# Kernel tuning notes

Measured on AMD Instinct MI355X. Metric: run time of the kernel, lower is better.

## Reference

```python
import jax, jax.numpy as jnp
import numpy as np

N = 8192      # num_nodes
B = 16        # batch
IN_DIM = 2    # input_dim
HID = 64      # hid_dim
K = 2         # diffusion_steps
DEG = 16
E = N * DEG
F = IN_DIM + HID            # concat(input, state) feature dim
NUM_MAT = 2 * K + 1         # dual random walk: 2 matrices * K steps + identity


def _spmm(vals, rows, cols, x):
    # sparse [N,N] @ dense [N,M]: y[rows[e]] += vals[e] * x[cols[e]]
    return jax.ops.segment_sum(vals[:, None] * x[cols], rows, num_segments=N)


def _diff_conv(x, W, b, edge_src, edge_dst, vals1, vals2):
    # x: [B, N, F] -> [B, N*out_dim]; Chebyshev-like diffusion recursion
    x0 = jnp.transpose(x, (1, 2, 0)).reshape(N, F * B)  # [N, F*B]
    xs = [x0]
    # matrix 1 = D_out^-1 A (edges src->dst), matrix 2 = D_in^-1 A^T (edges dst->src)
    for rows, cols, vals in ((edge_src, edge_dst, vals1), (edge_dst, edge_src, vals2)):
        x1 = _spmm(vals, rows, cols, x0)
        xs.append(x1)
        xp, xc = x0, x1
        for _ in range(2, K + 1):
            xn = 2.0 * _spmm(vals, rows, cols, xc) - xp
            xs.append(xn)
            xp, xc = xc, xn
    xstk = jnp.stack(xs, 0).reshape(NUM_MAT, N, F, B)
    xstk = jnp.transpose(xstk, (3, 1, 2, 0)).reshape(B * N, F * NUM_MAT)
    out = xstk @ W + b  # [B*N, out_dim]
    return out.reshape(B, -1)


def setup_inputs() -> dict:
    key = jax.random.key(0)
    k = jax.random.split(key, 8)
    inputs = jax.random.normal(k[0], (B, N * IN_DIM), jnp.float32)
    state = jax.random.normal(k[1], (B, N * HID), jnp.float32)
    edge_src = jax.random.randint(k[2], (E,), 0, N)
    edge_dst = jax.random.randint(k[3], (E,), 0, N)
    a = jax.random.uniform(k[4], (E,), jnp.float32) + 0.1  # positive edge weights
    dout = jax.ops.segment_sum(a, edge_src, num_segments=N)
    din = jax.ops.segment_sum(a, edge_dst, num_segments=N)
    vals1 = a / jnp.where(dout > 0, dout, 1.0)[edge_src]  # random-walk normalize A
    vals2 = a / jnp.where(din > 0, din, 1.0)[edge_dst]    # random-walk normalize A^T
    std_g = 1.414 * np.sqrt(2.0 / (F * NUM_MAT + 2 * HID)).astype(np.float32)
    std_c = 1.414 * np.sqrt(2.0 / (F * NUM_MAT + HID)).astype(np.float32)
    W_gate = jax.random.normal(k[5], (F * NUM_MAT, 2 * HID), jnp.float32) * std_g
    b_gate = jnp.zeros((2 * HID,), jnp.float32)
    W_cand = jax.random.normal(k[6], (F * NUM_MAT, HID), jnp.float32) * std_c
    b_cand = jnp.zeros((HID,), jnp.float32)
    return dict(inputs=inputs, state=state, edge_src=edge_src, edge_dst=edge_dst,
                vals1=vals1, vals2=vals2, W_gate=W_gate, b_gate=b_gate,
                W_cand=W_cand, b_cand=b_cand)


def reference(inputs, state, edge_src, edge_dst, vals1, vals2,
              W_gate, b_gate, W_cand, b_cand):
    i = inputs.reshape(B, N, IN_DIM)
    s = state.reshape(B, N, HID)
    x = jnp.concatenate([i, s], axis=2)  # [B, N, F]
    value = jax.nn.sigmoid(_diff_conv(x, W_gate, b_gate, edge_src, edge_dst, vals1, vals2))
    value = value.reshape(B, N, 2 * HID)
    r = value[..., :HID].reshape(B, N * HID)
    u = value[..., HID:].reshape(B, N * HID)
    rs = (r * state).reshape(B, N, HID)
    xc = jnp.concatenate([i, rs], axis=2)
    c = jnp.tanh(_diff_conv(xc, W_cand, b_cand, edge_src, edge_dst, vals1, vals2))
    new_state = u * state + (1.0 - u) * c
    return (new_state, new_state)
```

## Files before the change

kernel.cpp:

```cpp
#include <hip/hip_runtime.h>
#include <cstddef>
#include <cstdint>

#define NNODES 8192
#define BATCH  16
#define FDIM   66
#define HID    64
#define CCH    1056
#define NEDGE  131072
#define NFB    8650752
#define SN     524288
#define OUTHALF 8388608
#define KPAD   352
#define LDA    360
#define GN     8

typedef __attribute__((ext_vector_type(8))) short bf16x8;
typedef __attribute__((ext_vector_type(4))) float f32x4;

static __device__ __forceinline__ float bf2f(ushort u) {
    union { uint32_t i; float f; } c; c.i = ((uint32_t)u) << 16; return c.f;
}
static __device__ __forceinline__ ushort f2bf(float f) {
    union { float f; uint32_t i; } c; c.f = f;
    uint32_t lsb = (c.i >> 16) & 1;
    return (ushort)((c.i + 0x7fffu + lsb) >> 16);
}


__global__ void zero_counts_kernel(int* __restrict__ c1, int* __restrict__ c2) {
    int i = blockIdx.x * 256 + threadIdx.x;
    if (i < NNODES) { c1[i] = 0; c2[i] = 0; }
}

__global__ void hist_kernel(const int* __restrict__ src, const int* __restrict__ dst,
                            int* __restrict__ c1, int* __restrict__ c2) {
    int e = blockIdx.x * 256 + threadIdx.x;
    if (e < NEDGE) {
        atomicAdd(&c1[src[e]], 1);
        atomicAdd(&c2[dst[e]], 1);
    }
}

__global__ __launch_bounds__(1024) void scan_kernel(const int* __restrict__ counts,
                                                    int* __restrict__ rowptr,
                                                    int* __restrict__ cursor) {
    __shared__ int sh[1024];
    int tid = threadIdx.x;
    int base = tid * 8;
    int local[8];
    int sum = 0;
#pragma unroll
    for (int j = 0; j < 8; ++j) { local[j] = counts[base + j]; sum += local[j]; }
    sh[tid] = sum;
    __syncthreads();
    for (int off = 1; off < 1024; off <<= 1) {
        int v = (tid >= off) ? sh[tid - off] : 0;
        __syncthreads();
        sh[tid] += v;
        __syncthreads();
    }
    int p = sh[tid] - sum;
#pragma unroll
    for (int j = 0; j < 8; ++j) {
        cursor[base + j] = p;
        p += local[j];
        rowptr[base + j + 1] = p;
    }
    if (tid == 0) rowptr[0] = 0;
}

__global__ void scatter_kernel(const int* __restrict__ src, const int* __restrict__ dst,
                               const float* __restrict__ v1, const float* __restrict__ v2,
                               int* __restrict__ cur1, int* __restrict__ cur2,
                               int* __restrict__ cols1, float* __restrict__ valsC1,
                               int* __restrict__ cols2, float* __restrict__ valsC2) {
    int e = blockIdx.x * 256 + threadIdx.x;
    if (e < NEDGE) {
        int r1 = src[e];
        int p1 = atomicAdd(&cur1[r1], 1);
        cols1[p1] = dst[e];
        valsC1[p1] = v1[e];
        int r2 = dst[e];
        int p2 = atomicAdd(&cur2[r2], 1);
        cols2[p2] = src[e];
        valsC2[p2] = v2[e];
    }
}


__global__ void convert_w_kernel(const float* __restrict__ Wg, const float* __restrict__ Wc,
                                 ushort* __restrict__ WgT, ushort* __restrict__ WcT) {
    int i = blockIdx.x * 256 + threadIdx.x;
    if (i >= 192 * KPAD) return;
    int col = i / KPAD, kk = i - col * KPAD;
    if (col < 128) {
        WgT[col * KPAD + kk] = (kk < 330) ? f2bf(Wg[kk * 128 + col]) : (ushort)0;
    } else {
        int c = col - 128;
        WcT[c * KPAD + kk] = (kk < 330) ? f2bf(Wc[kk * 64 + c]) : (ushort)0;
    }
}


__global__ void build_x0_kernel(const float* __restrict__ inputs, const float* __restrict__ state,
                                ushort* __restrict__ X0) {
    int idx = blockIdx.x * 256 + threadIdx.x;
    if (idx >= NFB) return;
    int b = idx & 15;
    int t = idx >> 4;
    int f = t % FDIM;
    int n = t / FDIM;
    float v;
    if (f < 2) v = inputs[(size_t)b * (NNODES * 2) + n * 2 + f];
    else       v = state[(size_t)b * SN + n * HID + (f - 2)];
    X0[idx] = f2bf(v);
}


static __device__ __forceinline__ void fma8(float* acc, uint4 d, float v) {
    acc[0] += v * bf2f((ushort)(d.x));  acc[1] += v * bf2f((ushort)(d.x >> 16));
    acc[2] += v * bf2f((ushort)(d.y));  acc[3] += v * bf2f((ushort)(d.y >> 16));
    acc[4] += v * bf2f((ushort)(d.z));  acc[5] += v * bf2f((ushort)(d.z >> 16));
    acc[6] += v * bf2f((ushort)(d.w));  acc[7] += v * bf2f((ushort)(d.w >> 16));
}

static __device__ __forceinline__ uint4 blend_pack8(const float* acc, uint4 p,
                                                    float alpha, float beta) {
    float o[8];
    o[0] = alpha * acc[0] + beta * bf2f((ushort)(p.x));
    o[1] = alpha * acc[1] + beta * bf2f((ushort)(p.x >> 16));
    o[2] = alpha * acc[2] + beta * bf2f((ushort)(p.y));
    o[3] = alpha * acc[3] + beta * bf2f((ushort)(p.y >> 16));
    o[4] = alpha * acc[4] + beta * bf2f((ushort)(p.z));
    o[5] = alpha * acc[5] + beta * bf2f((ushort)(p.z >> 16));
    o[6] = alpha * acc[6] + beta * bf2f((ushort)(p.w));
    o[7] = alpha * acc[7] + beta * bf2f((ushort)(p.w >> 16));
    uint4 r;
    r.x = (uint32_t)f2bf(o[0]) | ((uint32_t)f2bf(o[1]) << 16);
    r.y = (uint32_t)f2bf(o[2]) | ((uint32_t)f2bf(o[3]) << 16);
    r.z = (uint32_t)f2bf(o[4]) | ((uint32_t)f2bf(o[5]) << 16);
    r.w = (uint32_t)f2bf(o[6]) | ((uint32_t)f2bf(o[7]) << 16);
    return r;
}

__global__ __launch_bounds__(128) void spmm_kernel(const int* __restrict__ rowptr,
                                                   const int* __restrict__ cols,
                                                   const float* __restrict__ vals,
                                                   const ushort* __restrict__ x,
                                                   const ushort* __restrict__ xp,
                                                   ushort* __restrict__ y,
                                                   float alpha, float beta) {
    int n = blockIdx.x;
    int t = threadIdx.x;
    int s = rowptr[n], e = rowptr[n + 1];
    float a0[8] = {0, 0, 0, 0, 0, 0, 0, 0};
    float a1[8] = {0, 0, 0, 0, 0, 0, 0, 0};
    bool tail = t < 4;
    for (int i = s; i < e; ++i) {
        float v = vals[i];
        int c = cols[i];
        const uint4* xb = (const uint4*)(x + (size_t)c * CCH);
        fma8(a0, xb[t], v);
        if (tail) fma8(a1, xb[128 + t], v);
    }
    uint4* yb = (uint4*)(y + (size_t)n * CCH);
    const uint4* xpb = (const uint4*)(xp + (size_t)n * CCH);
    uint4 p0 = (beta != 0.f) ? xpb[t] : make_uint4(0, 0, 0, 0);
    yb[t] = blend_pack8(a0, p0, alpha, beta);
    if (tail) {
        uint4 p1 = (beta != 0.f) ? xpb[128 + t] : make_uint4(0, 0, 0, 0);
        yb[128 + t] = blend_pack8(a1, p1, alpha, beta);
    }
}


__global__ __launch_bounds__(256) void gate_mfma(const ushort* __restrict__ Xb,
                                                 const ushort* __restrict__ WgT,
                                                 const float* __restrict__ bg,
                                                 const float* __restrict__ state,
                                                 float* __restrict__ U,
                                                 ushort* __restrict__ X0mut) {
    __shared__ __align__(16) ushort At[16 * LDA];
    int tid = threadIdx.x;
    int wave = tid >> 6, lane = tid & 63;
    int row = lane & 15, quad = lane >> 4;
    int c0 = (wave * 2) * 16 + row;
    int c1 = (wave * 2 + 1) * 16 + row;

    bf16x8 w0[11], w1[11];
#pragma unroll
    for (int k = 0; k < 11; ++k) {
        w0[k] = *(const bf16x8*)(WgT + (size_t)c0 * KPAD + k * 32 + quad * 8);
        w1[k] = *(const bf16x8*)(WgT + (size_t)c1 * KPAD + k * 32 + quad * 8);
    }
    float bias0 = bg[c0], bias1 = bg[c1];

    for (int p = tid; p < 16 * 22; p += 256) {
        int b = p / 22, kk = 330 + p % 22;
        At[b * LDA + kk] = 0;
    }

    int nodeBase = blockIdx.x * GN;
    for (int g = 0; g < GN; ++g) {
        int n = nodeBase + g;
        __syncthreads();
        for (int p = tid; p < 2640; p += 256) {
            int m = p / 528;
            int r2 = p - m * 528;
            int f = r2 >> 3;
            int bp = r2 & 7;
            uint d = *(const uint*)(Xb + (size_t)m * NFB + (size_t)n * CCH + f * 16 + bp * 2);
            int kk = f * 5 + m;
            int b = bp * 2;
            At[b * LDA + kk] = (ushort)d;
            At[(b + 1) * LDA + kk] = (ushort)(d >> 16);
        }
        __syncthreads();

        f32x4 acc0 = {0.f, 0.f, 0.f, 0.f};
        f32x4 acc1 = {0.f, 0.f, 0.f, 0.f};
#pragma unroll
        for (int k = 0; k < 11; ++k) {
            bf16x8 av = *(const bf16x8*)(At + row * LDA + k * 32 + quad * 8);
            acc0 = __builtin_amdgcn_mfma_f32_16x16x32_bf16(av, w0[k], acc0, 0, 0, 0);
            acc1 = __builtin_amdgcn_mfma_f32_16x16x32_bf16(av, w1[k], acc1, 0, 0, 0);
        }
#pragma unroll
        for (int r = 0; r < 4; ++r) {
            int b = quad * 4 + r;
            float v0 = 1.f / (1.f + __expf(-(acc0[r] + bias0)));
            float v1 = 1.f / (1.f + __expf(-(acc1[r] + bias1)));
            if (wave < 2) {
                float s0 = state[(size_t)b * SN + n * HID + c0];
                float s1 = state[(size_t)b * SN + n * HID + c1];
                X0mut[(size_t)n * CCH + (2 + c0) * 16 + b] = f2bf(v0 * s0);
                X0mut[(size_t)n * CCH + (2 + c1) * 16 + b] = f2bf(v1 * s1);
            } else {
                U[(size_t)b * SN + n * HID + (c0 - HID)] = v0;
                U[(size_t)b * SN + n * HID + (c1 - HID)] = v1;
            }
        }
    }
}


__global__ __launch_bounds__(256) void cand_mfma(const ushort* __restrict__ Xb,
                                                 const ushort* __restrict__ WcT,
                                                 const float* __restrict__ bc,
                                                 const float* __restrict__ state,
                                                 const float* __restrict__ U,
                                                 float* __restrict__ out) {
    __shared__ __align__(16) ushort At[16 * LDA];
    int tid = threadIdx.x;
    int wave = tid >> 6, lane = tid & 63;
    int row = lane & 15, quad = lane >> 4;
    int c = wave * 16 + row;

    bf16x8 w[11];
#pragma unroll
    for (int k = 0; k < 11; ++k)
        w[k] = *(const bf16x8*)(WcT + (size_t)c * KPAD + k * 32 + quad * 8);
    float bias = bc[c];

    for (int p = tid; p < 16 * 22; p += 256) {
        int b = p / 22, kk = 330 + p % 22;
        At[b * LDA + kk] = 0;
    }

    int nodeBase = blockIdx.x * GN;
    for (int g = 0; g < GN; ++g) {
        int n = nodeBase + g;
        __syncthreads();
        for (int p = tid; p < 2640; p += 256) {
            int m = p / 528;
            int r2 = p - m * 528;
            int f = r2 >> 3;
            int bp = r2 & 7;
            uint d = *(const uint*)(Xb + (size_t)m * NFB + (size_t)n * CCH + f * 16 + bp * 2);
            int kk = f * 5 + m;
            int b = bp * 2;
            At[b * LDA + kk] = (ushort)d;
            At[(b + 1) * LDA + kk] = (ushort)(d >> 16);
        }
        __syncthreads();

        f32x4 acc = {0.f, 0.f, 0.f, 0.f};
#pragma unroll
        for (int k = 0; k < 11; ++k) {
            bf16x8 av = *(const bf16x8*)(At + row * LDA + k * 32 + quad * 8);
            acc = __builtin_amdgcn_mfma_f32_16x16x32_bf16(av, w[k], acc, 0, 0, 0);
        }
#pragma unroll
        for (int r = 0; r < 4; ++r) {
            int b = quad * 4 + r;
            float pre = acc[r] + bias;
            float cv = 1.f - 2.f / (__expf(2.f * pre) + 1.f);
            size_t idx = (size_t)b * SN + n * HID + c;
            float uv = U[idx];
            float s = state[idx];
            float ns = uv * s + (1.f - uv) * cv;
            out[idx] = ns;
            out[OUTHALF + idx] = ns;
        }
    }
}


extern "C" void kernel_launch(void* const* d_in, const int* in_sizes, int n_in,
                              void* d_out, int out_size, void* d_ws, size_t ws_size,
                              hipStream_t stream) {
    const float* inputs = (const float*)d_in[0];
    const float* state  = (const float*)d_in[1];
    const int*   esrc   = (const int*)d_in[2];
    const int*   edst   = (const int*)d_in[3];
    const float* v1     = (const float*)d_in[4];
    const float* v2     = (const float*)d_in[5];
    const float* Wg     = (const float*)d_in[6];
    const float* bg     = (const float*)d_in[7];
    const float* Wc     = (const float*)d_in[8];
    const float* bc     = (const float*)d_in[9];
    float* out = (float*)d_out;

    char* ws = (char*)d_ws;
    size_t off = 0;
    auto alloc = [&](size_t bytes) -> void* {
        void* p = ws + off;
        off += (bytes + 255) & ~(size_t)255;
        return p;
    };
    ushort* Xb     = (ushort*)alloc((size_t)5 * NFB * 2);
    float*  U      = (float*)alloc((size_t)OUTHALF * 4);
    ushort* WgT    = (ushort*)alloc((size_t)128 * KPAD * 2);
    ushort* WcT    = (ushort*)alloc((size_t)64 * KPAD * 2);
    int*   counts1 = (int*)alloc(NNODES * 4);
    int*   counts2 = (int*)alloc(NNODES * 4);
    int*   rowptr1 = (int*)alloc((NNODES + 1) * 4);
    int*   rowptr2 = (int*)alloc((NNODES + 1) * 4);
    int*   cursor1 = (int*)alloc(NNODES * 4);
    int*   cursor2 = (int*)alloc(NNODES * 4);
    int*   cols1   = (int*)alloc(NEDGE * 4);
    int*   cols2   = (int*)alloc(NEDGE * 4);
    float* valsC1  = (float*)alloc(NEDGE * 4);
    float* valsC2  = (float*)alloc(NEDGE * 4);

    ushort* X0 = Xb;
    ushort* X1 = Xb + (size_t)1 * NFB;
    ushort* X2 = Xb + (size_t)2 * NFB;
    ushort* X3 = Xb + (size_t)3 * NFB;
    ushort* X4 = Xb + (size_t)4 * NFB;

    zero_counts_kernel<<<(NNODES + 255) / 256, 256, 0, stream>>>(counts1, counts2);
    hist_kernel<<<(NEDGE + 255) / 256, 256, 0, stream>>>(esrc, edst, counts1, counts2);
    scan_kernel<<<1, 1024, 0, stream>>>(counts1, rowptr1, cursor1);
    scan_kernel<<<1, 1024, 0, stream>>>(counts2, rowptr2, cursor2);
    scatter_kernel<<<(NEDGE + 255) / 256, 256, 0, stream>>>(esrc, edst, v1, v2,
                                                            cursor1, cursor2,
                                                            cols1, valsC1, cols2, valsC2);

    convert_w_kernel<<<(192 * KPAD + 255) / 256, 256, 0, stream>>>(Wg, Wc, WgT, WcT);
    build_x0_kernel<<<(NFB + 255) / 256, 256, 0, stream>>>(inputs, state, X0);

    spmm_kernel<<<NNODES, 128, 0, stream>>>(rowptr1, cols1, valsC1, X0, X0, X1, 1.f, 0.f);
    spmm_kernel<<<NNODES, 128, 0, stream>>>(rowptr1, cols1, valsC1, X1, X0, X2, 2.f, -1.f);
    spmm_kernel<<<NNODES, 128, 0, stream>>>(rowptr2, cols2, valsC2, X0, X0, X3, 1.f, 0.f);
    spmm_kernel<<<NNODES, 128, 0, stream>>>(rowptr2, cols2, valsC2, X3, X0, X4, 2.f, -1.f);

    gate_mfma<<<NNODES / GN, 256, 0, stream>>>(Xb, WgT, bg, state, U, X0);

    spmm_kernel<<<NNODES, 128, 0, stream>>>(rowptr1, cols1, valsC1, X0, X0, X1, 1.f, 0.f);
    spmm_kernel<<<NNODES, 128, 0, stream>>>(rowptr1, cols1, valsC1, X1, X0, X2, 2.f, -1.f);
    spmm_kernel<<<NNODES, 128, 0, stream>>>(rowptr2, cols2, valsC2, X0, X0, X3, 1.f, 0.f);
    spmm_kernel<<<NNODES, 128, 0, stream>>>(rowptr2, cols2, valsC2, X3, X0, X4, 2.f, -1.f);

    cand_mfma<<<NNODES / GN, 256, 0, stream>>>(Xb, WcT, bc, state, U, out);
}
```

Before: 628.2 us.

## Store diffusion features batch-major per node so MFMA reads operands directly

Reorders the diffusion feature storage into node-interleaved, batch-major slabs (feature dim padded to 72) and permutes the weight K order to match. The gate and candidate MFMA kernels can then load A fragments straight from global memory, dropping the LDS transpose and its barriers. It also unrolls the SpMM edge loop by two, adds a separate buffer for the reset-scaled state, and places the U buffer in the second half of the output. The cost is padding, which adds memory traffic (the SpMM tail now covers 16 threads instead of 4), and more complex indexing.

```diff
diff --git a/kernel.cpp b/kernel.cpp
--- a/kernel.cpp
+++ b/kernel.cpp
@@ -4,15 +4,16 @@
 
 #define NNODES 8192
 #define BATCH  16
-#define FDIM   66
 #define HID    64
-#define CCH    1056
 #define NEDGE  131072
-#define NFB    8650752
 #define SN     524288
 #define OUTHALF 8388608
-#define KPAD   352
-#define LDA    360
+#define FP2    72
+#define SLABU  1152
+#define NSTR   5760
+#define NSTR4  720
+#define XCS4   144
+#define KP2    384
 #define GN     8
 
 typedef __attribute__((ext_vector_type(8))) short bf16x8;
@@ -92,29 +93,41 @@
 __global__ void convert_w_kernel(const float* __restrict__ Wg, const float* __restrict__ Wc,
                                  ushort* __restrict__ WgT, ushort* __restrict__ WcT) {
     int i = blockIdx.x * 256 + threadIdx.x;
-    if (i >= 192 * KPAD) return;
-    int col = i / KPAD, kk = i - col * KPAD;
+    if (i >= 192 * KP2) return;
+    int col = i / KP2, k2 = i - col * KP2;
+    int m = k2 / FP2, f = k2 - m * FP2;
+    bool valid = (m < 5) && (f < 66);
+    int ko = f * 5 + m;
     if (col < 128) {
-        WgT[col * KPAD + kk] = (kk < 330) ? f2bf(Wg[kk * 128 + col]) : (ushort)0;
+        WgT[col * KP2 + k2] = valid ? f2bf(Wg[ko * 128 + col]) : (ushort)0;
     } else {
         int c = col - 128;
-        WcT[c * KPAD + kk] = (kk < 330) ? f2bf(Wc[kk * 64 + c]) : (ushort)0;
+        WcT[c * KP2 + k2] = valid ? f2bf(Wc[ko * 64 + c]) : (ushort)0;
     }
 }
 
 
 __global__ void build_x0_kernel(const float* __restrict__ inputs, const float* __restrict__ state,
-                                ushort* __restrict__ X0) {
-    int idx = blockIdx.x * 256 + threadIdx.x;
-    if (idx >= NFB) return;
-    int b = idx & 15;
-    int t = idx >> 4;
-    int f = t % FDIM;
-    int n = t / FDIM;
-    float v;
-    if (f < 2) v = inputs[(size_t)b * (NNODES * 2) + n * 2 + f];
-    else       v = state[(size_t)b * SN + n * HID + (f - 2)];
-    X0[idx] = f2bf(v);
+                                uint* __restrict__ Xb_u, uint* __restrict__ Xc_u) {
+    int t = blockIdx.x * 256 + threadIdx.x;
+    if (t >= NNODES * BATCH * 36) return;
+    int n = t / 576;
+    int r = t - n * 576;
+    int b = r / 36;
+    int j = r - b * 36;
+    int f0 = 2 * j;
+    uint val = 0;
+    if (f0 == 0) {
+        float v0 = inputs[(size_t)b * (NNODES * 2) + n * 2 + 0];
+        float v1 = inputs[(size_t)b * (NNODES * 2) + n * 2 + 1];
+        val = (uint)f2bf(v0) | ((uint)f2bf(v1) << 16);
+    } else if (f0 < 66) {
+        float v0 = state[(size_t)b * SN + n * HID + (f0 - 2)];
+        float v1 = state[(size_t)b * SN + n * HID + (f0 - 1)];
+        val = (uint)f2bf(v0) | ((uint)f2bf(v1) << 16);
+    }
+    Xb_u[(size_t)n * 2880 + r] = val;
+    if (f0 == 0 || f0 >= 66) Xc_u[t] = val;
 }
 
 
@@ -147,84 +160,96 @@
 __global__ __launch_bounds__(128) void spmm_kernel(const int* __restrict__ rowptr,
                                                    const int* __restrict__ cols,
                                                    const float* __restrict__ vals,
-                                                   const ushort* __restrict__ x,
-                                                   const ushort* __restrict__ xp,
-                                                   ushort* __restrict__ y,
+                                                   const uint4* __restrict__ x, int xs,
+                                                   const uint4* __restrict__ xp, int ps,
+                                                   uint4* __restrict__ y, int ys,
                                                    float alpha, float beta) {
     int n = blockIdx.x;
     int t = threadIdx.x;
     int s = rowptr[n], e = rowptr[n + 1];
     float a0[8] = {0, 0, 0, 0, 0, 0, 0, 0};
     float a1[8] = {0, 0, 0, 0, 0, 0, 0, 0};
-    bool tail = t < 4;
-    for (int i = s; i < e; ++i) {
-        float v = vals[i];
-        int c = cols[i];
-        const uint4* xb = (const uint4*)(x + (size_t)c * CCH);
-        fma8(a0, xb[t], v);
-        if (tail) fma8(a1, xb[128 + t], v);
-    }
-    uint4* yb = (uint4*)(y + (size_t)n * CCH);
-    const uint4* xpb = (const uint4*)(xp + (size_t)n * CCH);
+    bool tail = t < 16;
+    int t2 = 128 + t;
+    int i = s;
+    for (; i + 2 <= e; i += 2) {
+        int cA = cols[i], cB = cols[i + 1];
+        float vA = vals[i], vB = vals[i + 1];
+        const uint4* rA = x + (size_t)cA * xs;
+        const uint4* rB = x + (size_t)cB * xs;
+        uint4 dA = rA[t];
+        uint4 dB = rB[t];
+        uint4 dA1, dB1;
+        if (tail) { dA1 = rA[t2]; dB1 = rB[t2]; }
+        fma8(a0, dA, vA); fma8(a0, dB, vB);
+        if (tail) { fma8(a1, dA1, vA); fma8(a1, dB1, vB); }
+    }
+    if (i < e) {
+        int cA = cols[i];
+        float vA = vals[i];
+        const uint4* rA = x + (size_t)cA * xs;
+        uint4 dA = rA[t];
+        if (tail) { uint4 dA1 = rA[t2]; fma8(a1, dA1, vA); }
+        fma8(a0, dA, vA);
+    }
+    uint4* yb = y + (size_t)n * ys;
+    const uint4* xpb = xp + (size_t)n * ps;
     uint4 p0 = (beta != 0.f) ? xpb[t] : make_uint4(0, 0, 0, 0);
     yb[t] = blend_pack8(a0, p0, alpha, beta);
     if (tail) {
-        uint4 p1 = (beta != 0.f) ? xpb[128 + t] : make_uint4(0, 0, 0, 0);
-        yb[128 + t] = blend_pack8(a1, p1, alpha, beta);
-    }
-}
-
-
-__global__ __launch_bounds__(256) void gate_mfma(const ushort* __restrict__ Xb,
-                                                 const ushort* __restrict__ WgT,
-                                                 const float* __restrict__ bg,
-                                                 const float* __restrict__ state,
-                                                 float* __restrict__ U,
-                                                 ushort* __restrict__ X0mut) {
-    __shared__ __align__(16) ushort At[16 * LDA];
+        uint4 p1 = (beta != 0.f) ? xpb[t2] : make_uint4(0, 0, 0, 0);
+        yb[t2] = blend_pack8(a1, p1, alpha, beta);
+    }
+}
+
+
+__global__ __launch_bounds__(256, 2) void gate_mfma(const ushort* __restrict__ Xb,
+                                                    const ushort* __restrict__ WgT,
+                                                    const float* __restrict__ bg,
+                                                    const float* __restrict__ state,
+                                                    float* __restrict__ U,
+                                                    ushort* __restrict__ Xc) {
     int tid = threadIdx.x;
     int wave = tid >> 6, lane = tid & 63;
     int row = lane & 15, quad = lane >> 4;
-    int c0 = (wave * 2) * 16 + row;
-    int c1 = (wave * 2 + 1) * 16 + row;
-
-    bf16x8 w0[11], w1[11];
-#pragma unroll
-    for (int k = 0; k < 11; ++k) {
-        w0[k] = *(const bf16x8*)(WgT + (size_t)c0 * KPAD + k * 32 + quad * 8);
-        w1[k] = *(const bf16x8*)(WgT + (size_t)c1 * KPAD + k * 32 + quad * 8);
+    int c0 = wave * 32 + row;
+    int c1 = c0 + 16;
+
+    bf16x8 w0[12], w1[12];
+#pragma unroll
+    for (int kt = 0; kt < 12; ++kt) {
+        w0[kt] = *(const bf16x8*)(WgT + (size_t)c0 * KP2 + kt * 32 + quad * 8);
+        w1[kt] = *(const bf16x8*)(WgT + (size_t)c1 * KP2 + kt * 32 + quad * 8);
     }
     float bias0 = bg[c0], bias1 = bg[c1];
 
-    for (int p = tid; p < 16 * 22; p += 256) {
-        int b = p / 22, kk = 330 + p % 22;
-        At[b * LDA + kk] = 0;
-    }
+    int offA[11];
+#pragma unroll
+    for (int kt = 0; kt < 11; ++kt) {
+        int j = 4 * kt + quad;
+        int m = j / 9;
+        int f0 = 8 * (j - 9 * m);
+        offA[kt] = m * SLABU + row * FP2 + f0;
+    }
+    int off11 = 4 * SLABU + row * FP2 + 64;
 
     int nodeBase = blockIdx.x * GN;
     for (int g = 0; g < GN; ++g) {
         int n = nodeBase + g;
-        __syncthreads();
-        for (int p = tid; p < 2640; p += 256) {
-            int m = p / 528;
-            int r2 = p - m * 528;
-            int f = r2 >> 3;
-            int bp = r2 & 7;
-            uint d = *(const uint*)(Xb + (size_t)m * NFB + (size_t)n * CCH + f * 16 + bp * 2);
-            int kk = f * 5 + m;
-            int b = bp * 2;
-            At[b * LDA + kk] = (ushort)d;
-            At[(b + 1) * LDA + kk] = (ushort)(d >> 16);
-        }
-        __syncthreads();
-
+        const ushort* An = Xb + (size_t)n * NSTR;
         f32x4 acc0 = {0.f, 0.f, 0.f, 0.f};
         f32x4 acc1 = {0.f, 0.f, 0.f, 0.f};
 #pragma unroll
-        for (int k = 0; k < 11; ++k) {
-            bf16x8 av = *(const bf16x8*)(At + row * LDA + k * 32 + quad * 8);
-            acc0 = __builtin_amdgcn_mfma_f32_16x16x32_bf16(av, w0[k], acc0, 0, 0, 0);
-            acc1 = __builtin_amdgcn_mfma_f32_16x16x32_bf16(av, w1[k], acc1, 0, 0, 0);
+        for (int kt = 0; kt < 11; ++kt) {
+            bf16x8 av = *(const bf16x8*)(An + offA[kt]);
+            acc0 = __builtin_amdgcn_mfma_f32_16x16x32_bf16(av, w0[kt], acc0, 0, 0, 0);
+            acc1 = __builtin_amdgcn_mfma_f32_16x16x32_bf16(av, w1[kt], acc1, 0, 0, 0);
+        }
+        {
+            bf16x8 av = {0, 0, 0, 0, 0, 0, 0, 0};
+            if (quad == 0) av = *(const bf16x8*)(An + off11);
+            acc0 = __builtin_amdgcn_mfma_f32_16x16x32_bf16(av, w0[11], acc0, 0, 0, 0);
+            acc1 = __builtin_amdgcn_mfma_f32_16x16x32_bf16(av, w1[11], acc1, 0, 0, 0);
         }
 #pragma unroll
         for (int r = 0; r < 4; ++r) {
@@ -234,8 +259,8 @@
             if (wave < 2) {
                 float s0 = state[(size_t)b * SN + n * HID + c0];
                 float s1 = state[(size_t)b * SN + n * HID + c1];
-                X0mut[(size_t)n * CCH + (2 + c0) * 16 + b] = f2bf(v0 * s0);
-                X0mut[(size_t)n * CCH + (2 + c1) * 16 + b] = f2bf(v1 * s1);
+                Xc[(size_t)n * SLABU + b * FP2 + 2 + c0] = f2bf(v0 * s0);
+                Xc[(size_t)n * SLABU + b * FP2 + 2 + c1] = f2bf(v1 * s1);
             } else {
                 U[(size_t)b * SN + n * HID + (c0 - HID)] = v0;
                 U[(size_t)b * SN + n * HID + (c1 - HID)] = v1;
@@ -245,51 +270,51 @@
 }
 
 
-__global__ __launch_bounds__(256) void cand_mfma(const ushort* __restrict__ Xb,
-                                                 const ushort* __restrict__ WcT,
-                                                 const float* __restrict__ bc,
-                                                 const float* __restrict__ state,
-                                                 const float* __restrict__ U,
-                                                 float* __restrict__ out) {
-    __shared__ __align__(16) ushort At[16 * LDA];
+__global__ __launch_bounds__(256, 3) void cand_mfma(const ushort* __restrict__ Xb,
+                                                    const ushort* __restrict__ Xc,
+                                                    const ushort* __restrict__ WcT,
+                                                    const float* __restrict__ bc,
+                                                    const float* __restrict__ state,
+                                                    const float* U,
+                                                    float* out) {
     int tid = threadIdx.x;
     int wave = tid >> 6, lane = tid & 63;
     int row = lane & 15, quad = lane >> 4;
     int c = wave * 16 + row;
 
-    bf16x8 w[11];
-#pragma unroll
-    for (int k = 0; k < 11; ++k)
-        w[k] = *(const bf16x8*)(WcT + (size_t)c * KPAD + k * 32 + quad * 8);
+    bf16x8 w[12];
+#pragma unroll
+    for (int kt = 0; kt < 12; ++kt)
+        w[kt] = *(const bf16x8*)(WcT + (size_t)c * KP2 + kt * 32 + quad * 8);
     float bias = bc[c];
 
-    for (int p = tid; p < 16 * 22; p += 256) {
-        int b = p / 22, kk = 330 + p % 22;
-        At[b * LDA + kk] = 0;
-    }
+    int offA[11];
+#pragma unroll
+    for (int kt = 0; kt < 11; ++kt) {
+        int j = 4 * kt + quad;
+        int m = j / 9;
+        int f0 = 8 * (j - 9 * m);
+        offA[kt] = m * SLABU + row * FP2 + f0;
+    }
+    int off11 = 4 * SLABU + row * FP2 + 64;
 
     int nodeBase = blockIdx.x * GN;
     for (int g = 0; g < GN; ++g) {
         int n = nodeBase + g;
-        __syncthreads();
-        for (int p = tid; p < 2640; p += 256) {
-            int m = p / 528;
-            int r2 = p - m * 528;
-            int f = r2 >> 3;
-            int bp = r2 & 7;
-            uint d = *(const uint*)(Xb + (size_t)m * NFB + (size_t)n * CCH + f * 16 + bp * 2);
-            int kk = f * 5 + m;
-            int b = bp * 2;
-            At[b * LDA + kk] = (ushort)d;
-            At[(b + 1) * LDA + kk] = (ushort)(d >> 16);
-        }
-        __syncthreads();
-
+        const ushort* AnB = Xb + (size_t)n * NSTR;
+        const ushort* AnC = Xc + (size_t)n * SLABU;
         f32x4 acc = {0.f, 0.f, 0.f, 0.f};
 #pragma unroll
-        for (int k = 0; k < 11; ++k) {
-            bf16x8 av = *(const bf16x8*)(At + row * LDA + k * 32 + quad * 8);
-            acc = __builtin_amdgcn_mfma_f32_16x16x32_bf16(av, w[k], acc, 0, 0, 0);
+        for (int kt = 0; kt < 11; ++kt) {
+            const ushort* bp = (kt < 2) ? AnC
+                             : (kt == 2 ? (quad == 0 ? AnC : AnB) : AnB);
+            bf16x8 av = *(const bf16x8*)(bp + offA[kt]);
+            acc = __builtin_amdgcn_mfma_f32_16x16x32_bf16(av, w[kt], acc, 0, 0, 0);
+        }
+        {
+            bf16x8 av = {0, 0, 0, 0, 0, 0, 0, 0};
+            if (quad == 0) av = *(const bf16x8*)(AnB + off11);
+            acc = __builtin_amdgcn_mfma_f32_16x16x32_bf16(av, w[11], acc, 0, 0, 0);
         }
 #pragma unroll
         for (int r = 0; r < 4; ++r) {
@@ -329,10 +354,10 @@
         off += (bytes + 255) & ~(size_t)255;
         return p;
     };
-    ushort* Xb     = (ushort*)alloc((size_t)5 * NFB * 2);
-    float*  U      = (float*)alloc((size_t)OUTHALF * 4);
-    ushort* WgT    = (ushort*)alloc((size_t)128 * KPAD * 2);
-    ushort* WcT    = (ushort*)alloc((size_t)64 * KPAD * 2);
+    ushort* Xb     = (ushort*)alloc((size_t)NNODES * NSTR * 2);
+    ushort* Xc     = (ushort*)alloc((size_t)NNODES * SLABU * 2);
+    ushort* WgT    = (ushort*)alloc((size_t)128 * KP2 * 2);
+    ushort* WcT    = (ushort*)alloc((size_t)64 * KP2 * 2);
     int*   counts1 = (int*)alloc(NNODES * 4);
     int*   counts2 = (int*)alloc(NNODES * 4);
     int*   rowptr1 = (int*)alloc((NNODES + 1) * 4);
@@ -344,11 +369,11 @@
     float* valsC1  = (float*)alloc(NEDGE * 4);
     float* valsC2  = (float*)alloc(NEDGE * 4);
 
-    ushort* X0 = Xb;
-    ushort* X1 = Xb + (size_t)1 * NFB;
-    ushort* X2 = Xb + (size_t)2 * NFB;
-    ushort* X3 = Xb + (size_t)3 * NFB;
-    ushort* X4 = Xb + (size_t)4 * NFB;
+    float* U = out + OUTHALF;
+
+    uint4* Xb4 = (uint4*)Xb;
+    uint4* Xc4 = (uint4*)Xc;
+    auto slab = [&](int m) { return Xb4 + (size_t)m * 144; };
 
     zero_counts_kernel<<<(NNODES + 255) / 256, 256, 0, stream>>>(counts1, counts2);
     hist_kernel<<<(NEDGE + 255) / 256, 256, 0, stream>>>(esrc, edst, counts1, counts2);
@@ -358,20 +383,29 @@
                                                             cursor1, cursor2,
                                                             cols1, valsC1, cols2, valsC2);
 
-    convert_w_kernel<<<(192 * KPAD + 255) / 256, 256, 0, stream>>>(Wg, Wc, WgT, WcT);
-    build_x0_kernel<<<(NFB + 255) / 256, 256, 0, stream>>>(inputs, state, X0);
-
-    spmm_kernel<<<NNODES, 128, 0, stream>>>(rowptr1, cols1, valsC1, X0, X0, X1, 1.f, 0.f);
-    spmm_kernel<<<NNODES, 128, 0, stream>>>(rowptr1, cols1, valsC1, X1, X0, X2, 2.f, -1.f);
-    spmm_kernel<<<NNODES, 128, 0, stream>>>(rowptr2, cols2, valsC2, X0, X0, X3, 1.f, 0.f);
-    spmm_kernel<<<NNODES, 128, 0, stream>>>(rowptr2, cols2, valsC2, X3, X0, X4, 2.f, -1.f);
-
-    gate_mfma<<<NNODES / GN, 256, 0, stream>>>(Xb, WgT, bg, state, U, X0);
-
-    spmm_kernel<<<NNODES, 128, 0, stream>>>(rowptr1, cols1, valsC1, X0, X0, X1, 1.f, 0.f);
-    spmm_kernel<<<NNODES, 128, 0, stream>>>(rowptr1, cols1, valsC1, X1, X0, X2, 2.f, -1.f);
-    spmm_kernel<<<NNODES, 128, 0, stream>>>(rowptr2, cols2, valsC2, X0, X0, X3, 1.f, 0.f);
-    spmm_kernel<<<NNODES, 128, 0, stream>>>(rowptr2, cols2, valsC2, X3, X0, X4, 2.f, -1.f);
-
-    cand_mfma<<<NNODES / GN, 256, 0, stream>>>(Xb, WcT, bc, state, U, out);
-}
+    convert_w_kernel<<<(192 * KP2 + 255) / 256, 256, 0, stream>>>(Wg, Wc, WgT, WcT);
+    build_x0_kernel<<<(NNODES * BATCH * 36 + 255) / 256, 256, 0, stream>>>(
+        inputs, state, (uint*)Xb, (uint*)Xc);
+
+    spmm_kernel<<<NNODES, 128, 0, stream>>>(rowptr1, cols1, valsC1, slab(0), NSTR4,
+                                            slab(0), NSTR4, slab(1), NSTR4, 1.f, 0.f);
+    spmm_kernel<<<NNODES, 128, 0, stream>>>(rowptr1, cols1, valsC1, slab(1), NSTR4,
+                                            slab(0), NSTR4, slab(2), NSTR4, 2.f, -1.f);
+    spmm_kernel<<<NNODES, 128, 0, stream>>>(rowptr2, cols2, valsC2, slab(0), NSTR4,
+                                            slab(0), NSTR4, slab(3), NSTR4, 1.f, 0.f);
+    spmm_kernel<<<NNODES, 128, 0, stream>>>(rowptr2, cols2, valsC2, slab(3), NSTR4,
+                                            slab(0), NSTR4, slab(4), NSTR4, 2.f, -1.f);
+
+    gate_mfma<<<NNODES / GN, 256, 0, stream>>>(Xb, WgT, bg, state, U, Xc);
+
+    spmm_kernel<<<NNODES, 128, 0, stream>>>(rowptr1, cols1, valsC1, Xc4, XCS4,
+                                            Xc4, XCS4, slab(1), NSTR4, 1.f, 0.f);
+    spmm_kernel<<<NNODES, 128, 0, stream>>>(rowptr1, cols1, valsC1, slab(1), NSTR4,
+                                            Xc4, XCS4, slab(2), NSTR4, 2.f, -1.f);
+    spmm_kernel<<<NNODES, 128, 0, stream>>>(rowptr2, cols2, valsC2, Xc4, XCS4,
+                                            Xc4, XCS4, slab(3), NSTR4, 1.f, 0.f);
+    spmm_kernel<<<NNODES, 128, 0, stream>>>(rowptr2, cols2, valsC2, slab(3), NSTR4,
+                                            Xc4, XCS4, slab(4), NSTR4, 2.f, -1.f);
+
+    cand_mfma<<<NNODES / GN, 256, 0, stream>>>(Xb, Xc, WcT, bc, state, U, out);
+}
```

New measurement: 610.4 us. 2.8% less time.
